# Kernel optimization log

Hardware: AMD Instinct MI355X
Metric: run time of the kernel (lower is better)

The kernel has to match this reference:

```python
import jax, jax.numpy as jnp
import numpy as np

B, C, W, H = 4, 256, 64, 64
DK = 32


def setup_inputs() -> dict:
    key = jax.random.key(0)
    ks = jax.random.split(key, 5)
    x = jax.random.normal(ks[0], (B, C, W, H), dtype=jnp.float32)
    # 1x1 conv weights ~ linear projections; scale like conv default init
    s = 1.0 / np.sqrt(C)
    Wq = jax.random.normal(ks[1], (DK, C), dtype=jnp.float32) * s
    Wk = jax.random.normal(ks[2], (DK, C), dtype=jnp.float32) * s
    Wv = jax.random.normal(ks[3], (C, C), dtype=jnp.float32) * s
    bq = jnp.zeros((DK,), jnp.float32)
    bk = jnp.zeros((DK,), jnp.float32)
    bv = jnp.zeros((C,), jnp.float32)
    # NOTE: module initializes gamma=0 (output == x, zero grads to Q/K/V);
    # use a nonzero value so the attention path is exercised.
    gamma = jax.random.uniform(ks[4], (1,), dtype=jnp.float32) + 0.5
    return {"x": x, "Wq": Wq, "bq": bq, "Wk": Wk, "bk": bk,
            "Wv": Wv, "bv": bv, "gamma": gamma}


def reference(x, Wq, bq, Wk, bk, Wv, bv, gamma):
    b, c, w, h = x.shape
    n = w * h
    xf = x.reshape(b, c, n)                      # [B, C, N]
    q = jnp.einsum('kc,bcn->bkn', Wq, xf) + bq[None, :, None]  # [B, dk, N]
    k = jnp.einsum('kc,bcn->bkn', Wk, xf) + bk[None, :, None]  # [B, dk, N]
    v = jnp.einsum('oc,bcn->bon', Wv, xf) + bv[None, :, None]  # [B, C, N]
    energy = jnp.einsum('bkn,bkm->bnm', q, k)    # [B, N, N] (no 1/sqrt(dk) scale)
    attn = jax.nn.softmax(energy, axis=-1)       # softmax over keys m
    # out[b,c,n] = sum_m v[b,c,m] * attn[b,n,m]  (bmm(V, A^T))
    out = jnp.einsum('bcm,bnm->bcn', v, attn)
    out = out.reshape(b, c, w, h)
    out = gamma[0] * out + x                      # channel_in == channel_out
    return out
```

## Files before the change

kernel.cpp:

```cpp
#include <hip/hip_runtime.h>
#include <hip/hip_bf16.h>
#include <stdint.h>

typedef float f32x16 __attribute__((ext_vector_type(16)));
typedef short bf16x8 __attribute__((ext_vector_type(8)));

#define L2E 1.4426950408889634f
#define ROWPAT(r, hi) (((r) & 3) + 8 * ((r) >> 2) + 4 * (hi))

#define WCATB_OFF 0u
#define XT_OFF    163840u
#define QBUF_OFF  8552448u
#define KBUF_OFF  9601024u
#define VBUF_OFF  10649600u

static __device__ __forceinline__ ushort f2bf(float f) {
    union { float f; uint32_t u; } v; v.f = f;
    uint32_t u = v.u;
    return (ushort)((u + 0x7fffu + ((u >> 16) & 1u)) >> 16);
}

static __device__ __forceinline__ uint32_t cvtpk(float lo, float hi) {
    uint32_t r;
    asm volatile("v_cvt_pk_bf16_f32 %0, %1, %2" : "=v"(r) : "v"(lo), "v"(hi));
    return r;
}
static __device__ __forceinline__ bf16x8 packP(float p0, float p1, float p2, float p3,
                                               float p4, float p5, float p6, float p7) {
    uint32_t a0 = cvtpk(p0, p1), a1 = cvtpk(p2, p3);
    uint32_t b0 = cvtpk(p4, p5), b1 = cvtpk(p6, p7);
    auto s0 = __builtin_amdgcn_permlane32_swap(a0, b0, false, false);
    auto s1 = __builtin_amdgcn_permlane32_swap(a1, b1, false, false);
    union { uint32_t u[4]; bf16x8 v; } pk;
    pk.u[0] = s0[0];
    pk.u[1] = s1[0];
    pk.u[2] = s0[1];
    pk.u[3] = s1[1];
    return pk.v;
}

__global__ void prep_kernel(const float* __restrict__ Wq, const float* __restrict__ Wk,
                            const float* __restrict__ Wv, ushort* __restrict__ Wcb) {
    int row = blockIdx.x, c = threadIdx.x;
    float v;
    if (row < 32)      v = Wq[row * 256 + c];
    else if (row < 64) v = Wk[(row - 32) * 256 + c];
    else               v = Wv[(row - 64) * 256 + c];
    Wcb[row * 256 + c] = f2bf(v);
}

__global__ __launch_bounds__(256)
void xt_kernel(const float* __restrict__ x, ushort* __restrict__ xT) {
    __shared__ ushort t[64][80];
    const int tid = threadIdx.x;
    const int b = blockIdx.x >> 8;
    const int c0 = ((blockIdx.x >> 6) & 3) << 6;
    const int n0 = (blockIdx.x & 63) << 6;
    const float* xb = x + ((size_t)(b * 256 + c0)) * 4096 + n0;
    #pragma unroll
    for (int p = 0; p < 4; ++p) {
        int cl = (tid >> 4) + p * 16;
        int nl = (tid & 15) * 4;
        float4 v = *(const float4*)(xb + (size_t)cl * 4096 + nl);
        t[nl + 0][cl] = f2bf(v.x);
        t[nl + 1][cl] = f2bf(v.y);
        t[nl + 2][cl] = f2bf(v.z);
        t[nl + 3][cl] = f2bf(v.w);
    }
    __syncthreads();
    ushort* xo = xT + ((size_t)(b * 4096 + n0)) * 256 + c0;
    #pragma unroll
    for (int p = 0; p < 2; ++p) {
        int idx = tid + (p << 8);
        int nl = idx >> 3, sg = idx & 7;
        *(uint4*)(xo + (size_t)nl * 256 + sg * 8) = *(const uint4*)&t[nl][sg * 8];
    }
}

__global__ __launch_bounds__(256)
void proj_qk_kernel(const ushort* __restrict__ xT, const ushort* __restrict__ Wcb,
                    const float* __restrict__ bq, const float* __restrict__ bk,
                    ushort* __restrict__ qbuf, ushort* __restrict__ kbuf) {
    const int tid = threadIdx.x;
    const int w = tid >> 6, l31 = tid & 31, hi = (tid & 63) >> 5;
    const int b = blockIdx.x >> 6;
    const int nt = (blockIdx.x & 63) * 2 + (w & 1);
    const int isK = w >> 1;

    const ushort* xrow = xT + ((size_t)(b * 4096 + nt * 32 + l31)) * 256;
    const ushort* wrow = Wcb + (size_t)(isK * 32 + l31) * 256;

    f32x16 acc = (f32x16)0.0f;
    #pragma unroll
    for (int kk = 0; kk < 16; ++kk) {
        bf16x8 af = *(const bf16x8*)&xrow[kk * 16 + hi * 8];
        bf16x8 bf8 = *(const bf16x8*)&wrow[kk * 16 + hi * 8];
        acc = __builtin_amdgcn_mfma_f32_32x32x16_bf16(af, bf8, acc, 0, 0, 0);
    }
    const float bias = isK ? bk[l31] : bq[l31];
    const float scale = isK ? 1.0f : L2E;
    ushort* dst = isK ? kbuf : qbuf;
    #pragma unroll
    for (int r = 0; r < 16; ++r) {
        int n = nt * 32 + ROWPAT(r, hi);
        dst[((size_t)((b << 12) + n)) * 32 + l31] = f2bf((acc[r] + bias) * scale);
    }
}

__global__ __launch_bounds__(256)
void proj_v_kernel(const ushort* __restrict__ xT, const ushort* __restrict__ Wcb,
                   const float* __restrict__ bv, ushort* __restrict__ vbuf) {
    const int tid = threadIdx.x;
    const int w = tid >> 6, l31 = tid & 31, hi = (tid & 63) >> 5;
    const int b = blockIdx.x >> 8;
    const int ct = (blockIdx.x >> 5) & 7;
    const int nt = (blockIdx.x & 31) * 4 + w;

    const ushort* wv = Wcb + (size_t)(64 + ct * 32 + l31) * 256;
    const ushort* xrow = xT + ((size_t)(b * 4096 + nt * 32 + l31)) * 256;

    f32x16 acc = (f32x16)0.0f;
    #pragma unroll
    for (int kk = 0; kk < 16; ++kk) {
        bf16x8 af = *(const bf16x8*)&wv[kk * 16 + hi * 8];
        bf16x8 bf8 = *(const bf16x8*)&xrow[kk * 16 + hi * 8];
        acc = __builtin_amdgcn_mfma_f32_32x32x16_bf16(af, bf8, acc, 0, 0, 0);
    }
    #pragma unroll
    for (int r = 0; r < 16; ++r) {
        int c = ct * 32 + ROWPAT(r, hi);
        vbuf[((size_t)(b * 256 + c)) * 4096 + nt * 32 + l31] = f2bf(acc[r] + bv[c]);
    }
}

#define KSTR 36
#define VSTR 66
__global__ __launch_bounds__(256, 2)
void attn_kernel(const ushort* __restrict__ qbuf, const ushort* __restrict__ kbuf,
                 const ushort* __restrict__ vbuf, const float* __restrict__ x,
                 const float* __restrict__ gammap, float* __restrict__ out) {
    __shared__ ushort klds[2][64 * KSTR];
    __shared__ ushort vlds[2][256 * VSTR];
    __shared__ float  dlds[2][32];

    const int tid = threadIdx.x;
    const int bid = blockIdx.x;
    const int work = (bid & 7) * 64 + (bid >> 3);
    const int b = work >> 7;
    const int qbase = (work & 127) << 5;
    const int w = tid >> 6, l = tid & 63;
    const int l31 = l & 31, hi = l >> 5;
    const int kh = w >> 1, cp = w & 1;

    const ushort* kb = kbuf + ((size_t)b << 12) * 32;
    const ushort* vb = vbuf + ((size_t)b << 8) * 4096;

    const ushort* qrow = qbuf + ((size_t)((b << 12) + qbase + l31)) * 32;
    const bf16x8 qf0 = *(const bf16x8*)&qrow[hi * 8];
    const bf16x8 qf1 = *(const bf16x8*)&qrow[16 + hi * 8];

    f32x16 acc[4];
    #pragma unroll
    for (int ch = 0; ch < 4; ++ch) acc[ch] = (f32x16)0.0f;
    float dsum = 0.f;

    const int vc = tid >> 3, vs = tid & 7;
    const int krow = tid >> 2, kseg = tid & 3;
    const ushort* vsrc = vb + (size_t)vc * 4096 + vs * 8;
    const ushort* ksrc = kb + (size_t)krow * 32 + kseg * 8;
    uint4 vreg[8], kreg;

    #pragma unroll
    for (int i = 0; i < 8; ++i)
        vreg[i] = *(const uint4*)(vsrc + (size_t)i * 32 * 4096);
    kreg = *(const uint4*)ksrc;
    #pragma unroll
    for (int i = 0; i < 8; ++i)
        *(uint4*)&vlds[0][(vc + 32 * i) * VSTR + vs * 8] = vreg[i];
    *(uint4*)&klds[0][krow * KSTR + kseg * 8] = kreg;
    __syncthreads();

    for (int it = 0; it < 64; ++it) {
        const int cur = it & 1;
        if (it < 63) {
            const size_t m0 = (size_t)(it + 1) << 6;
            #pragma unroll
            for (int i = 0; i < 8; ++i)
                vreg[i] = *(const uint4*)(vsrc + (size_t)i * 32 * 4096 + m0);
            kreg = *(const uint4*)(ksrc + (m0 << 5));
        }

        const int krow_a = (kh * 32 + l31) * KSTR;
        bf16x8 kf0 = *(const bf16x8*)&klds[cur][krow_a + hi * 8];
        bf16x8 kf1 = *(const bf16x8*)&klds[cur][krow_a + 16 + hi * 8];
        f32x16 sT = __builtin_amdgcn_mfma_f32_32x32x16_bf16(kf0, qf0, (f32x16)0.0f, 0, 0, 0);
        sT = __builtin_amdgcn_mfma_f32_32x32x16_bf16(kf1, qf1, sT, 0, 0, 0);

        float p[16];
        #pragma unroll
        for (int r = 0; r < 16; ++r) {
            p[r] = exp2f(sT[r]);
            dsum += p[r];
        }
        bf16x8 pf0 = packP(p[0], p[1], p[2], p[3], p[4], p[5], p[6], p[7]);
        bf16x8 pf1 = packP(p[8], p[9], p[10], p[11], p[12], p[13], p[14], p[15]);

        __builtin_amdgcn_s_setprio(1);
        #pragma unroll
        for (int ch = 0; ch < 4; ++ch) {
            const int crow = (cp * 128 + ch * 32 + l31) * VSTR + kh * 32;
            bf16x8 vfa = *(const bf16x8*)&vlds[cur][crow + hi * 8];
            bf16x8 vfb = *(const bf16x8*)&vlds[cur][crow + 16 + hi * 8];
            acc[ch] = __builtin_amdgcn_mfma_f32_32x32x16_bf16(vfa, pf0, acc[ch], 0, 0, 0);
            acc[ch] = __builtin_amdgcn_mfma_f32_32x32x16_bf16(vfb, pf1, acc[ch], 0, 0, 0);
        }
        __builtin_amdgcn_s_setprio(0);

        if (it < 63) {
            const int nb = cur ^ 1;
            #pragma unroll
            for (int i = 0; i < 8; ++i)
                *(uint4*)&vlds[nb][(vc + 32 * i) * VSTR + vs * 8] = vreg[i];
            *(uint4*)&klds[nb][krow * KSTR + kseg * 8] = kreg;
        }
        __syncthreads();
    }

    const float gam = gammap[0];
    float dall = dsum + __shfl_xor(dsum, 32);
    float* scr = (float*)&vlds[0][0];
    if (kh == 1) {
        #pragma unroll
        for (int ch = 0; ch < 4; ++ch)
            #pragma unroll
            for (int r = 0; r < 16; ++r)
                scr[(((cp * 4 + ch) * 16 + r) << 6) + l] = acc[ch][r];
    }
    if (cp == 0 && l < 32) dlds[kh][l31] = dall;
    __syncthreads();
    if (kh == 0) {
        const float denom = dlds[0][l31] + dlds[1][l31];
        const float ginv = gam / denom;
        const float* xb2 = x + (((size_t)b) << 8) * 4096;
        float* ob = out + (((size_t)b) << 8) * 4096;
        const int q = qbase + l31;
        #pragma unroll
        for (int ch = 0; ch < 4; ++ch) {
            #pragma unroll
            for (int r = 0; r < 16; ++r) {
                int c = cp * 128 + ch * 32 + ROWPAT(r, hi);
                float o = acc[ch][r] + scr[(((cp * 4 + ch) * 16 + r) << 6) + l];
                size_t idx = (size_t)c * 4096 + q;
                ob[idx] = o * ginv + xb2[idx];
            }
        }
    }
}

extern "C" void kernel_launch(void* const* d_in, const int* in_sizes, int n_in,
                              void* d_out, int out_size, void* d_ws, size_t ws_size,
                              hipStream_t stream) {
    (void)in_sizes; (void)n_in; (void)out_size; (void)ws_size;
    const float* x     = (const float*)d_in[0];
    const float* Wq    = (const float*)d_in[1];
    const float* bq    = (const float*)d_in[2];
    const float* Wk    = (const float*)d_in[3];
    const float* bk    = (const float*)d_in[4];
    const float* Wv    = (const float*)d_in[5];
    const float* bv    = (const float*)d_in[6];
    const float* gamma = (const float*)d_in[7];
    float* out = (float*)d_out;

    char* ws = (char*)d_ws;
    ushort* Wcb  = (ushort*)(ws + WCATB_OFF);
    ushort* xT   = (ushort*)(ws + XT_OFF);
    ushort* qbuf = (ushort*)(ws + QBUF_OFF);
    ushort* kbuf = (ushort*)(ws + KBUF_OFF);
    ushort* vbuf = (ushort*)(ws + VBUF_OFF);

    prep_kernel<<<320, 256, 0, stream>>>(Wq, Wk, Wv, Wcb);
    xt_kernel<<<1024, 256, 0, stream>>>(x, xT);
    proj_qk_kernel<<<256, 256, 0, stream>>>(xT, Wcb, bq, bk, qbuf, kbuf);
    proj_v_kernel<<<1024, 256, 0, stream>>>(xT, Wcb, bv, vbuf);
    attn_kernel<<<512, 256, 0, stream>>>(qbuf, kbuf, vbuf, x, gamma, out);
}
```

Measured before the change: 121.2 us.

## Fuse transpose and QKV projections into one kernel; repartition attention PV work

Replaces the separate x-transpose, QK projection and V projection kernels with one kernel that transposes a 32-column tile of x into shared memory and computes Q, K and V from it. This removes the xT round trip through global memory and two kernel launches. The attention kernel also changes its work split: each wave now owns half of the softmax rows for its key half across all 256 channels (8 accumulators, one MFMA each) rather than all rows for half the channels. The epilogue gains a multi-stage shared-memory reduction with extra barriers, and the larger accumulator set raises register pressure.

```diff
diff --git a/kernel.cpp b/kernel.cpp
--- a/kernel.cpp
+++ b/kernel.cpp
@@ -9,10 +9,9 @@
 #define ROWPAT(r, hi) (((r) & 3) + 8 * ((r) >> 2) + 4 * (hi))
 
 #define WCATB_OFF 0u
-#define XT_OFF    163840u
-#define QBUF_OFF  8552448u
-#define KBUF_OFF  9601024u
-#define VBUF_OFF  10649600u
+#define QBUF_OFF  163840u
+#define KBUF_OFF  1212416u
+#define VBUF_OFF  2260992u
 
 static __device__ __forceinline__ ushort f2bf(float f) {
     union { float f; uint32_t u; } v; v.f = f;
@@ -50,86 +49,64 @@
 }
 
 __global__ __launch_bounds__(256)
-void xt_kernel(const float* __restrict__ x, ushort* __restrict__ xT) {
-    __shared__ ushort t[64][80];
+void fproj_kernel(const float* __restrict__ x, const ushort* __restrict__ Wcb,
+                  const float* __restrict__ bq, const float* __restrict__ bk,
+                  const float* __restrict__ bv,
+                  ushort* __restrict__ qbuf, ushort* __restrict__ kbuf,
+                  ushort* __restrict__ vbuf) {
+    __shared__ ushort xt[32 * 264];
     const int tid = threadIdx.x;
-    const int b = blockIdx.x >> 8;
-    const int c0 = ((blockIdx.x >> 6) & 3) << 6;
-    const int n0 = (blockIdx.x & 63) << 6;
-    const float* xb = x + ((size_t)(b * 256 + c0)) * 4096 + n0;
-    #pragma unroll
-    for (int p = 0; p < 4; ++p) {
-        int cl = (tid >> 4) + p * 16;
-        int nl = (tid & 15) * 4;
-        float4 v = *(const float4*)(xb + (size_t)cl * 4096 + nl);
-        t[nl + 0][cl] = f2bf(v.x);
-        t[nl + 1][cl] = f2bf(v.y);
-        t[nl + 2][cl] = f2bf(v.z);
-        t[nl + 3][cl] = f2bf(v.w);
-    }
-    __syncthreads();
-    ushort* xo = xT + ((size_t)(b * 4096 + n0)) * 256 + c0;
-    #pragma unroll
-    for (int p = 0; p < 2; ++p) {
-        int idx = tid + (p << 8);
-        int nl = idx >> 3, sg = idx & 7;
-        *(uint4*)(xo + (size_t)nl * 256 + sg * 8) = *(const uint4*)&t[nl][sg * 8];
-    }
-}
-
-__global__ __launch_bounds__(256)
-void proj_qk_kernel(const ushort* __restrict__ xT, const ushort* __restrict__ Wcb,
-                    const float* __restrict__ bq, const float* __restrict__ bk,
-                    ushort* __restrict__ qbuf, ushort* __restrict__ kbuf) {
-    const int tid = threadIdx.x;
-    const int w = tid >> 6, l31 = tid & 31, hi = (tid & 63) >> 5;
-    const int b = blockIdx.x >> 6;
-    const int nt = (blockIdx.x & 63) * 2 + (w & 1);
-    const int isK = w >> 1;
-
-    const ushort* xrow = xT + ((size_t)(b * 4096 + nt * 32 + l31)) * 256;
-    const ushort* wrow = Wcb + (size_t)(isK * 32 + l31) * 256;
-
-    f32x16 acc = (f32x16)0.0f;
-    #pragma unroll
-    for (int kk = 0; kk < 16; ++kk) {
-        bf16x8 af = *(const bf16x8*)&xrow[kk * 16 + hi * 8];
-        bf16x8 bf8 = *(const bf16x8*)&wrow[kk * 16 + hi * 8];
-        acc = __builtin_amdgcn_mfma_f32_32x32x16_bf16(af, bf8, acc, 0, 0, 0);
-    }
-    const float bias = isK ? bk[l31] : bq[l31];
-    const float scale = isK ? 1.0f : L2E;
-    ushort* dst = isK ? kbuf : qbuf;
-    #pragma unroll
-    for (int r = 0; r < 16; ++r) {
-        int n = nt * 32 + ROWPAT(r, hi);
-        dst[((size_t)((b << 12) + n)) * 32 + l31] = f2bf((acc[r] + bias) * scale);
-    }
-}
-
-__global__ __launch_bounds__(256)
-void proj_v_kernel(const ushort* __restrict__ xT, const ushort* __restrict__ Wcb,
-                   const float* __restrict__ bv, ushort* __restrict__ vbuf) {
-    const int tid = threadIdx.x;
-    const int w = tid >> 6, l31 = tid & 31, hi = (tid & 63) >> 5;
-    const int b = blockIdx.x >> 8;
-    const int ct = (blockIdx.x >> 5) & 7;
-    const int nt = (blockIdx.x & 31) * 4 + w;
-
-    const ushort* wv = Wcb + (size_t)(64 + ct * 32 + l31) * 256;
-    const ushort* xrow = xT + ((size_t)(b * 4096 + nt * 32 + l31)) * 256;
-
-    f32x16 acc = (f32x16)0.0f;
-    #pragma unroll
-    for (int kk = 0; kk < 16; ++kk) {
-        bf16x8 af = *(const bf16x8*)&wv[kk * 16 + hi * 8];
-        bf16x8 bf8 = *(const bf16x8*)&xrow[kk * 16 + hi * 8];
-        acc = __builtin_amdgcn_mfma_f32_32x32x16_bf16(af, bf8, acc, 0, 0, 0);
-    }
-    #pragma unroll
-    for (int r = 0; r < 16; ++r) {
-        int c = ct * 32 + ROWPAT(r, hi);
-        vbuf[((size_t)(b * 256 + c)) * 4096 + nt * 32 + l31] = f2bf(acc[r] + bv[c]);
+    const int b = blockIdx.x >> 7;
+    const int n0 = (blockIdx.x & 127) << 5;
+
+    const float* xb = x + (((size_t)b) << 20) + n0;
+    #pragma unroll
+    for (int i = 0; i < 8; ++i) {
+        int task = tid + (i << 8);
+        int c = task >> 3, seg = task & 7;
+        float4 v = *(const float4*)(xb + (size_t)c * 4096 + seg * 4);
+        xt[(seg * 4 + 0) * 264 + c] = f2bf(v.x);
+        xt[(seg * 4 + 1) * 264 + c] = f2bf(v.y);
+        xt[(seg * 4 + 2) * 264 + c] = f2bf(v.z);
+        xt[(seg * 4 + 3) * 264 + c] = f2bf(v.w);
+    }
+    __syncthreads();
+
+    const int w = tid >> 6, l = tid & 63;
+    const int l31 = l & 31, hi = l >> 5;
+
+    for (int cc = w; cc < 10; cc += 4) {
+        const int wbase = (cc < 2) ? cc * 32 : (cc - 2) * 32 + 64;
+        const ushort* wrow = Wcb + (size_t)(wbase + l31) * 256;
+        f32x16 acc = (f32x16)0.0f;
+        if (cc < 2) {
+            #pragma unroll
+            for (int kk = 0; kk < 16; ++kk) {
+                bf16x8 xf = *(const bf16x8*)&xt[l31 * 264 + kk * 16 + hi * 8];
+                bf16x8 wf = *(const bf16x8*)&wrow[kk * 16 + hi * 8];
+                acc = __builtin_amdgcn_mfma_f32_32x32x16_bf16(xf, wf, acc, 0, 0, 0);
+            }
+            const float bias = (cc == 0) ? bq[l31] : bk[l31];
+            const float scale = (cc == 0) ? L2E : 1.0f;
+            ushort* dst = (cc == 0) ? qbuf : kbuf;
+            #pragma unroll
+            for (int r = 0; r < 16; ++r) {
+                int n = n0 + ROWPAT(r, hi);
+                dst[((size_t)((b << 12) + n)) * 32 + l31] = f2bf((acc[r] + bias) * scale);
+            }
+        } else {
+            #pragma unroll
+            for (int kk = 0; kk < 16; ++kk) {
+                bf16x8 wf = *(const bf16x8*)&wrow[kk * 16 + hi * 8];
+                bf16x8 xf = *(const bf16x8*)&xt[l31 * 264 + kk * 16 + hi * 8];
+                acc = __builtin_amdgcn_mfma_f32_32x32x16_bf16(wf, xf, acc, 0, 0, 0);
+            }
+            #pragma unroll
+            for (int r = 0; r < 16; ++r) {
+                int c = (wbase - 64) + ROWPAT(r, hi);
+                vbuf[((size_t)(b * 256 + c)) * 4096 + n0 + l31] = f2bf(acc[r] + bv[c]);
+            }
+        }
     }
 }
 
@@ -141,7 +118,7 @@
                  const float* __restrict__ gammap, float* __restrict__ out) {
     __shared__ ushort klds[2][64 * KSTR];
     __shared__ ushort vlds[2][256 * VSTR];
-    __shared__ float  dlds[2][32];
+    __shared__ float  dlds[2][2][32];
 
     const int tid = threadIdx.x;
     const int bid = blockIdx.x;
@@ -151,6 +128,7 @@
     const int w = tid >> 6, l = tid & 63;
     const int l31 = l & 31, hi = l >> 5;
     const int kh = w >> 1, cp = w & 1;
+    const int cps = __builtin_amdgcn_readfirstlane(cp);
 
     const ushort* kb = kbuf + ((size_t)b << 12) * 32;
     const ushort* vb = vbuf + ((size_t)b << 8) * 4096;
@@ -159,9 +137,9 @@
     const bf16x8 qf0 = *(const bf16x8*)&qrow[hi * 8];
     const bf16x8 qf1 = *(const bf16x8*)&qrow[16 + hi * 8];
 
-    f32x16 acc[4];
-    #pragma unroll
-    for (int ch = 0; ch < 4; ++ch) acc[ch] = (f32x16)0.0f;
+    f32x16 acc[8];
+    #pragma unroll
+    for (int ch = 0; ch < 8; ++ch) acc[ch] = (f32x16)0.0f;
     float dsum = 0.f;
 
     const int vc = tid >> 3, vs = tid & 7;
@@ -180,6 +158,9 @@
     *(uint4*)&klds[0][krow * KSTR + kseg * 8] = kreg;
     __syncthreads();
 
+    const int vcol = kh * 32 + cp * 16 + hi * 8;
+    const int krow_a = (kh * 32 + l31) * KSTR;
+
     for (int it = 0; it < 64; ++it) {
         const int cur = it & 1;
         if (it < 63) {
@@ -190,29 +171,27 @@
             kreg = *(const uint4*)(ksrc + (m0 << 5));
         }
 
-        const int krow_a = (kh * 32 + l31) * KSTR;
         bf16x8 kf0 = *(const bf16x8*)&klds[cur][krow_a + hi * 8];
         bf16x8 kf1 = *(const bf16x8*)&klds[cur][krow_a + 16 + hi * 8];
         f32x16 sT = __builtin_amdgcn_mfma_f32_32x32x16_bf16(kf0, qf0, (f32x16)0.0f, 0, 0, 0);
         sT = __builtin_amdgcn_mfma_f32_32x32x16_bf16(kf1, qf1, sT, 0, 0, 0);
 
-        float p[16];
-        #pragma unroll
-        for (int r = 0; r < 16; ++r) {
-            p[r] = exp2f(sT[r]);
-            dsum += p[r];
-        }
-        bf16x8 pf0 = packP(p[0], p[1], p[2], p[3], p[4], p[5], p[6], p[7]);
-        bf16x8 pf1 = packP(p[8], p[9], p[10], p[11], p[12], p[13], p[14], p[15]);
+        float p[8];
+        if (cps) {
+            p[0] = exp2f(sT[8]);  p[1] = exp2f(sT[9]);  p[2] = exp2f(sT[10]); p[3] = exp2f(sT[11]);
+            p[4] = exp2f(sT[12]); p[5] = exp2f(sT[13]); p[6] = exp2f(sT[14]); p[7] = exp2f(sT[15]);
+        } else {
+            p[0] = exp2f(sT[0]);  p[1] = exp2f(sT[1]);  p[2] = exp2f(sT[2]);  p[3] = exp2f(sT[3]);
+            p[4] = exp2f(sT[4]);  p[5] = exp2f(sT[5]);  p[6] = exp2f(sT[6]);  p[7] = exp2f(sT[7]);
+        }
+        dsum += ((p[0] + p[1]) + (p[2] + p[3])) + ((p[4] + p[5]) + (p[6] + p[7]));
+        bf16x8 pf = packP(p[0], p[1], p[2], p[3], p[4], p[5], p[6], p[7]);
 
         __builtin_amdgcn_s_setprio(1);
         #pragma unroll
-        for (int ch = 0; ch < 4; ++ch) {
-            const int crow = (cp * 128 + ch * 32 + l31) * VSTR + kh * 32;
-            bf16x8 vfa = *(const bf16x8*)&vlds[cur][crow + hi * 8];
-            bf16x8 vfb = *(const bf16x8*)&vlds[cur][crow + 16 + hi * 8];
-            acc[ch] = __builtin_amdgcn_mfma_f32_32x32x16_bf16(vfa, pf0, acc[ch], 0, 0, 0);
-            acc[ch] = __builtin_amdgcn_mfma_f32_32x32x16_bf16(vfb, pf1, acc[ch], 0, 0, 0);
+        for (int ch = 0; ch < 8; ++ch) {
+            bf16x8 vfa = *(const bf16x8*)&vlds[cur][(ch * 32 + l31) * VSTR + vcol];
+            acc[ch] = __builtin_amdgcn_mfma_f32_32x32x16_bf16(vfa, pf, acc[ch], 0, 0, 0);
         }
         __builtin_amdgcn_s_setprio(0);
 
@@ -228,31 +207,57 @@
 
     const float gam = gammap[0];
     float dall = dsum + __shfl_xor(dsum, 32);
+    if (l < 32) dlds[kh][cp][l31] = dall;
     float* scr = (float*)&vlds[0][0];
+    __syncthreads();
     if (kh == 1) {
         #pragma unroll
-        for (int ch = 0; ch < 4; ++ch)
+        for (int ch = 0; ch < 8; ++ch)
             #pragma unroll
             for (int r = 0; r < 16; ++r)
-                scr[(((cp * 4 + ch) * 16 + r) << 6) + l] = acc[ch][r];
-    }
-    if (cp == 0 && l < 32) dlds[kh][l31] = dall;
+                scr[(((cp * 8 + ch) * 16 + r) << 6) + l] = acc[ch][r];
+    }
     __syncthreads();
     if (kh == 0) {
-        const float denom = dlds[0][l31] + dlds[1][l31];
-        const float ginv = gam / denom;
-        const float* xb2 = x + (((size_t)b) << 8) * 4096;
-        float* ob = out + (((size_t)b) << 8) * 4096;
-        const int q = qbase + l31;
-        #pragma unroll
-        for (int ch = 0; ch < 4; ++ch) {
+        #pragma unroll
+        for (int ch = 0; ch < 8; ++ch)
+            #pragma unroll
+            for (int r = 0; r < 16; ++r)
+                acc[ch][r] += scr[(((cp * 8 + ch) * 16 + r) << 6) + l];
+    }
+    __syncthreads();
+    if (kh == 0 && cp == 1) {
+        #pragma unroll
+        for (int ch = 0; ch < 8; ++ch)
+            #pragma unroll
+            for (int r = 0; r < 16; ++r)
+                scr[((ch * 16 + r) << 6) + l] = acc[ch][r];
+    }
+    __syncthreads();
+    if (kh == 0 && cp == 0) {
+        #pragma unroll
+        for (int ch = 0; ch < 8; ++ch)
             #pragma unroll
             for (int r = 0; r < 16; ++r) {
-                int c = cp * 128 + ch * 32 + ROWPAT(r, hi);
-                float o = acc[ch][r] + scr[(((cp * 4 + ch) * 16 + r) << 6) + l];
-                size_t idx = (size_t)c * 4096 + q;
-                ob[idx] = o * ginv + xb2[idx];
-            }
+                float o = acc[ch][r] + scr[((ch * 16 + r) << 6) + l];
+                scr[((ch * 16 + r) << 6) + l] = o;
+            }
+    }
+    __syncthreads();
+    const float denom = dlds[0][0][l31] + dlds[0][1][l31] + dlds[1][0][l31] + dlds[1][1][l31];
+    const float ginv = gam / denom;
+    const float* xb2 = x + (((size_t)b) << 8) * 4096;
+    float* ob = out + (((size_t)b) << 8) * 4096;
+    const int q = qbase + l31;
+    #pragma unroll
+    for (int j = 0; j < 2; ++j) {
+        const int ch = w * 2 + j;
+        #pragma unroll
+        for (int r = 0; r < 16; ++r) {
+            int c = ch * 32 + ROWPAT(r, hi);
+            float o = scr[((ch * 16 + r) << 6) + l];
+            size_t idx = (size_t)c * 4096 + q;
+            ob[idx] = o * ginv + xb2[idx];
         }
     }
 }
@@ -273,14 +278,11 @@
 
     char* ws = (char*)d_ws;
     ushort* Wcb  = (ushort*)(ws + WCATB_OFF);
-    ushort* xT   = (ushort*)(ws + XT_OFF);
     ushort* qbuf = (ushort*)(ws + QBUF_OFF);
     ushort* kbuf = (ushort*)(ws + KBUF_OFF);
     ushort* vbuf = (ushort*)(ws + VBUF_OFF);
 
     prep_kernel<<<320, 256, 0, stream>>>(Wq, Wk, Wv, Wcb);
-    xt_kernel<<<1024, 256, 0, stream>>>(x, xT);
-    proj_qk_kernel<<<256, 256, 0, stream>>>(xT, Wcb, bq, bk, qbuf, kbuf);
-    proj_v_kernel<<<1024, 256, 0, stream>>>(xT, Wcb, bv, vbuf);
+    fproj_kernel<<<512, 256, 0, stream>>>(x, Wcb, bq, bk, bv, qbuf, kbuf, vbuf);
     attn_kernel<<<512, 256, 0, stream>>>(qbuf, kbuf, vbuf, x, gamma, out);
 }
```

Measured after the change: 112.0 us. 1.08x faster.
